# Kernel optimization log

Measured on AMD Instinct MI355X. Metric: run time of the kernel, lower is better.

## Reference

```python
import jax, jax.numpy as jnp
import numpy as np

NUM_EMBEDDINGS = 4096
EMBEDDING_DIM = 256
COMMITMENT_COST = 0.25
N_TOKENS = 32768


def setup_inputs() -> dict:
    key = jax.random.key(0)
    k1, k2 = jax.random.split(key)
    inputs = jax.random.normal(k1, (N_TOKENS, EMBEDDING_DIM), dtype=jnp.float32)
    # torch init: uniform(-1/K, 1/K)
    lim = 1.0 / NUM_EMBEDDINGS
    weight = jax.random.uniform(k2, (NUM_EMBEDDINGS, EMBEDDING_DIM), dtype=jnp.float32,
                                minval=-lim, maxval=lim)
    return {"inputs": inputs, "weight": weight}


def reference(inputs, weight):
    distances = (jnp.sum(inputs ** 2, axis=1, keepdims=True)
                 + jnp.sum(weight ** 2, axis=1)
                 - 2.0 * jnp.matmul(inputs, weight.T))
    encoding_indices = jnp.argmin(distances, axis=1)                       # [N]
    encodings = jax.nn.one_hot(encoding_indices, NUM_EMBEDDINGS,
                               dtype=jnp.float32)                          # [N, K]
    # gather replaces onehot @ weight (same values)
    quantized = weight[encoding_indices]                                   # [N, D]

    commitment_loss = jnp.mean((jax.lax.stop_gradient(quantized) - inputs) ** 2)
    codebook_loss = jnp.mean((quantized - jax.lax.stop_gradient(inputs)) ** 2)
    loss = codebook_loss + COMMITMENT_COST * commitment_loss

    # straight-through estimator
    quantized_st = inputs + jax.lax.stop_gradient(quantized - inputs)

    avg_probs = jnp.mean(encodings, axis=0)                                # [K]
    perplexity = jnp.exp(-jnp.sum(avg_probs * jnp.log(avg_probs + 1e-10)))

    return (quantized_st, perplexity, encodings, encoding_indices, loss)
```

## Files before the change

### kernel.cpp

```cpp
#include <hip/hip_runtime.h>

#define N_TOK 32768
#define N_EMB 4096
#define DIM 256

typedef short bf16x8 __attribute__((ext_vector_type(8)));
typedef float f32x4 __attribute__((ext_vector_type(4)));
typedef unsigned short us8 __attribute__((ext_vector_type(8)));


static __device__ __forceinline__ unsigned short f2bf(float f) {
    unsigned int u = __float_as_uint(f);
    u = (u + 0x7fffu + ((u >> 16) & 1u)) >> 16;
    return (unsigned short)u;
}

__device__ __forceinline__ float pw128_sq(const float4* a4) {
#pragma clang fp contract(off)
    float4 v0 = a4[0], v1 = a4[1];
    float r0 = v0.x * v0.x, r1 = v0.y * v0.y, r2 = v0.z * v0.z, r3 = v0.w * v0.w;
    float r4 = v1.x * v1.x, r5 = v1.y * v1.y, r6 = v1.z * v1.z, r7 = v1.w * v1.w;
    #pragma unroll
    for (int i = 1; i < 16; ++i) {
        v0 = a4[2 * i]; v1 = a4[2 * i + 1];
        float s;
        s = v0.x * v0.x; r0 += s;
        s = v0.y * v0.y; r1 += s;
        s = v0.z * v0.z; r2 += s;
        s = v0.w * v0.w; r3 += s;
        s = v1.x * v1.x; r4 += s;
        s = v1.y * v1.y; r5 += s;
        s = v1.z * v1.z; r6 += s;
        s = v1.w * v1.w; r7 += s;
    }
    return ((r0 + r1) + (r2 + r3)) + ((r4 + r5) + (r6 + r7));
}

__global__ __launch_bounds__(256) void k_norm_np(const float* __restrict__ src,
                                                 float* __restrict__ dst, int nrows) {
#pragma clang fp contract(off)
    int row = blockIdx.x * 256 + threadIdx.x;
    if (row >= nrows) return;
    const float4* a = (const float4*)(src + (size_t)row * DIM);
    float lo = pw128_sq(a);
    float hi = pw128_sq(a + 32);
    dst[row] = lo + hi;
}

__global__ __launch_bounds__(256) void k_shuf1(const float* __restrict__ src,
                                               unsigned short* __restrict__ hi) {
    int tid = blockIdx.x * 256 + threadIdx.x;
    int b = tid >> 6, lane = tid & 63;
    int T = b >> 3, C = b & 7;
    int row = T * 16 + (lane & 15);
    int col = C * 32 + (lane >> 4) * 8;
    const float* s = src + (size_t)row * DIM + col;
    us8 h;
    #pragma unroll
    for (int j = 0; j < 8; ++j) h[j] = f2bf(s[j]);
    *(us8*)(hi + (size_t)tid * 8) = h;
}

__global__ __launch_bounds__(256, 4) void k_score_mfma(
        const float* __restrict__ x, const float* __restrict__ w,
        const float* __restrict__ e2_np, const float* __restrict__ x2_np,
        const unsigned short* __restrict__ Xh,
        const unsigned short* __restrict__ Wh,
        float* __restrict__ out_idx, unsigned int* __restrict__ counts,
        float* enc,
        float* __restrict__ outq, float* __restrict__ loss_acc) {
    __shared__ __align__(16) short Abuf[8192];
    __shared__ float Tmax[4][32];
    __shared__ unsigned int ccnt[32];
    __shared__ int clist[32][16];
    __shared__ float Red_d[32 * 8];
    __shared__ int   Red_i[32 * 8];
    __shared__ float sred[4];

    const int t = threadIdx.x;
    const int wave = t >> 6, lane = t & 63;
    const int tok0 = blockIdx.x * 32;
    const int q = lane >> 4, c = lane & 15;

    #pragma unroll
    for (int i = 0; i < 4; ++i) {
        int idx = wave * 4 + i;
        int tile = idx >> 3, C = idx & 7;
        int Tg = blockIdx.x * 2 + tile;
        const unsigned short* src = Xh + ((size_t)(Tg * 8 + C) * 64 + lane) * 8;
        __builtin_amdgcn_global_load_lds(
            (const __attribute__((address_space(1))) unsigned int*)src,
            (__attribute__((address_space(3))) unsigned int*)(Abuf + idx * 512),
            16, 0, 0);
    }
    if (t < 32) ccnt[t] = 0;
    __syncthreads();

    f32x4* ez = enc ? (f32x4*)(enc + (size_t)tok0 * N_EMB) : (f32x4*)0;
    const f32x4 zf4 = {0.f, 0.f, 0.f, 0.f};

    float vmax[8], v2[8];
    #pragma unroll
    for (int s = 0; s < 8; ++s) { vmax[s] = -3.4e38f; v2[s] = -3.4e38f; }
    for (int jt = 0; jt < N_EMB; jt += 256) {
        const int U0 = (jt >> 4) + wave * 4;
        f32x4 acc[2][4] = {};
        #pragma unroll
        for (int C = 0; C < 8; ++C) {
            bf16x8 ah[2], bh[4];
            #pragma unroll
            for (int m = 0; m < 2; ++m)
                ah[m] = *(const bf16x8*)(Abuf + (size_t)(m * 8 + C) * 512 + lane * 8);
            #pragma unroll
            for (int n = 0; n < 4; ++n)
                bh[n] = *(const bf16x8*)(Wh + (((size_t)(U0 + n) * 8 + C) * 64 + lane) * 8);
            #pragma unroll
            for (int m = 0; m < 2; ++m)
                #pragma unroll
                for (int n = 0; n < 4; ++n)
                    acc[m][n] = __builtin_amdgcn_mfma_f32_16x16x32_bf16(ah[m], bh[n], acc[m][n], 0, 0, 0);
        }
        {
            unsigned int idb = ((unsigned int)jt >> 8) << 2;
            #pragma unroll
            for (int m = 0; m < 2; ++m)
                #pragma unroll
                for (int n = 0; n < 4; ++n)
                    #pragma unroll
                    for (int r = 0; r < 4; ++r) {
                        float p = __uint_as_float(
                            (__float_as_uint(acc[m][n][r]) & ~63u) | (idb + (unsigned)n));
                        int s = m * 4 + r;
                        if (p > vmax[s]) { v2[s] = vmax[s]; vmax[s] = p; }
                        else if (p > v2[s]) v2[s] = p;
                    }
        }
        if (ez) {
            int base = (jt >> 8) * 8 * 256 + t;
            #pragma unroll
            for (int j = 0; j < 8; ++j)
                __builtin_nontemporal_store(zf4, ez + base + j * 256);
        }
    }
    float rmax[8];
    #pragma unroll
    for (int s = 0; s < 8; ++s) rmax[s] = vmax[s];
    #pragma unroll
    for (int off = 1; off < 16; off <<= 1)
        #pragma unroll
        for (int s = 0; s < 8; ++s)
            rmax[s] = fmaxf(rmax[s], __shfl_xor(rmax[s], off));
    if (c == 0) {
        #pragma unroll
        for (int m = 0; m < 2; ++m)
            #pragma unroll
            for (int r = 0; r < 4; ++r)
                Tmax[wave][m * 16 + q * 4 + r] = rmax[m * 4 + r];
    }
    __syncthreads();
    if (t < 32) {
        float mx = fmaxf(fmaxf(Tmax[0][t], Tmax[1][t]),
                         fmaxf(Tmax[2][t], Tmax[3][t]));
        Tmax[0][t] = mx - 1.5e-4f;
    }
    __syncthreads();
    float thr[8];
    #pragma unroll
    for (int m = 0; m < 2; ++m)
        #pragma unroll
        for (int r = 0; r < 4; ++r)
            thr[m * 4 + r] = Tmax[0][m * 16 + q * 4 + r];

    #pragma unroll
    for (int s = 0; s < 8; ++s) {
        int m = s >> 2, r = s & 3;
        int tokl = m * 16 + q * 4 + r;
        #pragma unroll
        for (int h = 0; h < 2; ++h) {
            float pv = h ? v2[s] : vmax[s];
            if (pv >= thr[s]) {
                unsigned int id = __float_as_uint(pv) & 63u;
                int code = ((int)(id >> 2) * 16 + wave * 4 + (int)(id & 3u)) * 16 + c;
                unsigned int p = atomicAdd(&ccnt[tokl], 1u);
                if (p < 16) clist[tokl][p] = code;
            }
        }
    }
    __syncthreads();

    {
        int token = t >> 3, slot = t & 7;
        int cnt = (int)ccnt[token]; if (cnt > 16) cnt = 16;
        float bd = 3.4e38f;
        int bi = 0x7fffffff;
        float x2 = x2_np[tok0 + token];
        const float4* xr = (const float4*)(x + (size_t)(tok0 + token) * DIM);
        for (int k = slot; k < cnt; k += 8) {
            int code = clist[token][k];
            const float4* wr = (const float4*)(w + (size_t)code * DIM);
            double dot = 0.0;
            for (int g = 0; g < 64; ++g) {
                float4 xv = xr[g];
                float4 wv = wr[g];
                dot += (double)xv.x * (double)wv.x;
                dot += (double)xv.y * (double)wv.y;
                dot += (double)xv.z * (double)wv.z;
                dot += (double)xv.w * (double)wv.w;
            }
            {
#pragma clang fp contract(off)
                float M  = (float)dot;
                float S  = x2 + e2_np[code];
                float dd = S - 2.0f * M;
                if (dd < bd || (dd == bd && code < bi)) { bd = dd; bi = code; }
            }
        }
        Red_d[token * 8 + slot] = bd;
        Red_i[token * 8 + slot] = bi;
    }
    __syncthreads();
    if (t < 32) {
        float fv = Red_d[t * 8];
        int   fi = Red_i[t * 8];
        #pragma unroll
        for (int k = 1; k < 8; ++k) {
            float v = Red_d[t * 8 + k];
            int  ii = Red_i[t * 8 + k];
            if (v < fv || (v == fv && ii < fi)) { fv = v; fi = ii; }
        }
        out_idx[tok0 + t] = (float)fi;
        atomicAdd(&counts[fi], 1u);
        ccnt[t] = (unsigned int)fi;
    }
    __syncthreads();

    {
        int token = t >> 3, slot = t & 7;
        int fi = (int)ccnt[token];
        if (enc && slot == 0)
            __builtin_nontemporal_store(1.0f, enc + (size_t)(tok0 + token) * N_EMB + fi);
        const f32x4* wr = (const f32x4*)(w + (size_t)fi * DIM);
        const f32x4* xr = (const f32x4*)(x + (size_t)(tok0 + token) * DIM);
        f32x4* oq = (f32x4*)(outq + (size_t)(tok0 + token) * DIM);
        float sse = 0.f;
        #pragma unroll
        for (int g0 = 0; g0 < 8; ++g0) {
            int g = slot * 8 + g0;
            f32x4 qv = wr[g];
            f32x4 xv = xr[g];
            __builtin_nontemporal_store(qv, oq + g);
            float dx = qv.x - xv.x, dy = qv.y - xv.y;
            float dz = qv.z - xv.z, dw = qv.w - xv.w;
            sse += dx * dx + dy * dy + dz * dz + dw * dw;
        }
        #pragma unroll
        for (int off = 32; off > 0; off >>= 1) sse += __shfl_down(sse, off, 64);
        if (lane == 0) sred[wave] = sse;
    }
    __syncthreads();
    if (t == 0)
        atomicAdd(loss_acc, sred[0] + sred[1] + sred[2] + sred[3]);
}

__global__ __launch_bounds__(256) void k_onehot(const float* __restrict__ out_idx,
                                                float* __restrict__ enc) {
    int token = blockIdx.x;
    int idx = (int)out_idx[token];
    float4* row = (float4*)(enc + (size_t)token * N_EMB);
    #pragma unroll
    for (int p = 0; p < 4; ++p) {
        int g = threadIdx.x + 256 * p;
        float4 v = make_float4(0.f, 0.f, 0.f, 0.f);
        int d0 = g * 4;
        if (idx >= d0 && idx < d0 + 4) ((float*)&v)[idx - d0] = 1.0f;
        row[g] = v;
    }
}

__global__ __launch_bounds__(256) void k_final(const unsigned int* __restrict__ counts,
                                               const float* __restrict__ loss_acc,
                                               float* __restrict__ out_perp,
                                               float* __restrict__ out_loss) {
    __shared__ float sred[4];
    int t = threadIdx.x;
    float h = 0.f;
    for (int k = t; k < N_EMB; k += 256) {
        float p = (float)counts[k] * (1.0f / N_TOK);
        h += p * logf(p + 1e-10f);
    }
    #pragma unroll
    for (int off = 32; off > 0; off >>= 1) h += __shfl_down(h, off, 64);
    if ((t & 63) == 0) sred[t >> 6] = h;
    __syncthreads();
    if (t == 0) {
        float s = sred[0] + sred[1] + sred[2] + sred[3];
        *out_perp = expf(-s);
        *out_loss = loss_acc[0] * 1.25f / 8388608.0f;
    }
}

extern "C" void kernel_launch(void* const* d_in, const int* in_sizes, int n_in,
                              void* d_out, int out_size, void* d_ws, size_t ws_size,
                              hipStream_t stream) {
    const float* x = (const float*)d_in[0];
    const float* w = (const float*)d_in[1];
    float* out  = (float*)d_out;
    float* out0 = out;
    float* out1 = out0 + 8388608;
    float* out2 = out1 + 1;
    float* out3 = out2 + 134217728;
    float* out4 = out3 + 32768;

    unsigned int* counts = (unsigned int*)d_ws;
    float* loss_acc = (float*)((char*)d_ws + 16384);
    float* e2_np    = (float*)((char*)d_ws + 16896);
    float* x2_np    = (float*)((char*)d_ws + 33280);

    bool big_ws = ws_size >= (size_t)(20u * 1024u * 1024u);
    unsigned short *Xh, *Wh;
    float* enc_arg;
    if (big_ws) {
        Xh = (unsigned short*)((char*)d_ws + (1u << 20));
        Wh = Xh + 8388608;
        enc_arg = out2;
    } else {
        uintptr_t sb = ((uintptr_t)out2 + 255) & ~(uintptr_t)255;
        Xh = (unsigned short*)sb;
        Wh = Xh + 8388608;
        enc_arg = nullptr;
    }

    hipMemsetAsync(d_ws, 0, 16640, stream);
    k_norm_np<<<N_EMB / 256, 256, 0, stream>>>(w, e2_np, N_EMB);
    k_norm_np<<<N_TOK / 256, 256, 0, stream>>>(x, x2_np, N_TOK);
    k_shuf1<<<N_TOK * DIM / 8 / 256, 256, 0, stream>>>(x, Xh);
    k_shuf1<<<N_EMB * DIM / 8 / 256, 256, 0, stream>>>(w, Wh);
    k_score_mfma<<<N_TOK / 32, 256, 0, stream>>>(x, w, e2_np, x2_np, Xh, Wh,
                                                 out3, counts, enc_arg,
                                                 out0, loss_acc);
    if (!big_ws)
        k_onehot<<<N_TOK, 256, 0, stream>>>(out3, out2);
    k_final<<<1, 256, 0, stream>>>(counts, loss_acc, out1, out4);
}
```

Measured before the change: 756.5 us.

## Fuse prep kernels, branchless top-2 tracking, move one-hot zeroing after scoring

Merges the two norm kernels and two bf16 shuffle kernels into one prep launch that converts a 16-row tile and computes the row norms in the same block. Replaces the per-element branchy top-2 update in the score loop with a branchless fmax/fmed3 network over four candidates at once. Moves the non-temporal zero stores of the one-hot output out of the MFMA loop into one burst after candidate selection. This trades launch overhead and branch divergence for some loss of overlap between the zeroing stores and the matrix work.

```diff
diff --git a/kernel.cpp b/kernel.cpp
--- a/kernel.cpp
+++ b/kernel.cpp
@@ -13,6 +13,10 @@
     unsigned int u = __float_as_uint(f);
     u = (u + 0x7fffu + ((u >> 16) & 1u)) >> 16;
     return (unsigned short)u;
+}
+
+static __device__ __forceinline__ float pkid(float x, unsigned int id) {
+    return __uint_as_float((__float_as_uint(x) & ~63u) | id);
 }
 
 __device__ __forceinline__ float pw128_sq(const float4* a4) {
@@ -36,29 +40,38 @@
     return ((r0 + r1) + (r2 + r3)) + ((r4 + r5) + (r6 + r7));
 }
 
-__global__ __launch_bounds__(256) void k_norm_np(const float* __restrict__ src,
-                                                 float* __restrict__ dst, int nrows) {
-#pragma clang fp contract(off)
-    int row = blockIdx.x * 256 + threadIdx.x;
-    if (row >= nrows) return;
-    const float4* a = (const float4*)(src + (size_t)row * DIM);
-    float lo = pw128_sq(a);
-    float hi = pw128_sq(a + 32);
-    dst[row] = lo + hi;
-}
-
-__global__ __launch_bounds__(256) void k_shuf1(const float* __restrict__ src,
-                                               unsigned short* __restrict__ hi) {
-    int tid = blockIdx.x * 256 + threadIdx.x;
-    int b = tid >> 6, lane = tid & 63;
-    int T = b >> 3, C = b & 7;
-    int row = T * 16 + (lane & 15);
-    int col = C * 32 + (lane >> 4) * 8;
-    const float* s = src + (size_t)row * DIM + col;
-    us8 h;
-    #pragma unroll
-    for (int j = 0; j < 8; ++j) h[j] = f2bf(s[j]);
-    *(us8*)(hi + (size_t)tid * 8) = h;
+__global__ __launch_bounds__(256) void k_prep(const float* __restrict__ x,
+                                              const float* __restrict__ w,
+                                              unsigned short* __restrict__ Xh,
+                                              unsigned short* __restrict__ Wh,
+                                              float* __restrict__ x2_np,
+                                              float* __restrict__ e2_np) {
+    int bid = blockIdx.x;
+    const float* src;
+    unsigned short* dst;
+    float* ndst;
+    int T;
+    if (bid < N_TOK / 16) { src = x; dst = Xh; ndst = x2_np; T = bid; }
+    else                  { src = w; dst = Wh; ndst = e2_np; T = bid - N_TOK / 16; }
+    const int t = threadIdx.x, lane = t & 63, g = t >> 6;
+    #pragma unroll
+    for (int cc = 0; cc < 2; ++cc) {
+        int C = g * 2 + cc;
+        int row = T * 16 + (lane & 15);
+        int col = C * 32 + (lane >> 4) * 8;
+        const float* s = src + (size_t)row * DIM + col;
+        us8 h;
+        #pragma unroll
+        for (int j = 0; j < 8; ++j) h[j] = f2bf(s[j]);
+        *(us8*)(dst + ((size_t)(T * 8 + C) * 64 + lane) * 8) = h;
+    }
+    if (t < 16) {
+        int row = T * 16 + t;
+        const float4* a = (const float4*)(src + (size_t)row * DIM);
+        float lo = pw128_sq(a);
+        float hi = pw128_sq(a + 32);
+        ndst[row] = lo + hi;
+    }
 }
 
 __global__ __launch_bounds__(256, 4) void k_score_mfma(
@@ -96,9 +109,6 @@
     if (t < 32) ccnt[t] = 0;
     __syncthreads();
 
-    f32x4* ez = enc ? (f32x4*)(enc + (size_t)tok0 * N_EMB) : (f32x4*)0;
-    const f32x4 zf4 = {0.f, 0.f, 0.f, 0.f};
-
     float vmax[8], v2[8];
     #pragma unroll
     for (int s = 0; s < 8; ++s) { vmax[s] = -3.4e38f; v2[s] = -3.4e38f; }
@@ -125,21 +135,19 @@
             #pragma unroll
             for (int m = 0; m < 2; ++m)
                 #pragma unroll
-                for (int n = 0; n < 4; ++n)
-                    #pragma unroll
-                    for (int r = 0; r < 4; ++r) {
-                        float p = __uint_as_float(
-                            (__float_as_uint(acc[m][n][r]) & ~63u) | (idb + (unsigned)n));
-                        int s = m * 4 + r;
-                        if (p > vmax[s]) { v2[s] = vmax[s]; vmax[s] = p; }
-                        else if (p > v2[s]) v2[s] = p;
-                    }
-        }
-        if (ez) {
-            int base = (jt >> 8) * 8 * 256 + t;
-            #pragma unroll
-            for (int j = 0; j < 8; ++j)
-                __builtin_nontemporal_store(zf4, ez + base + j * 256);
+                for (int r = 0; r < 4; ++r) {
+                    int s = m * 4 + r;
+                    float p0 = pkid(acc[m][0][r], idb + 0);
+                    float p1 = pkid(acc[m][1][r], idb + 1);
+                    float p2 = pkid(acc[m][2][r], idb + 2);
+                    float p3 = pkid(acc[m][3][r], idb + 3);
+                    float t1a = fmaxf(fmaxf(vmax[s], p0), p1);
+                    float t2a = __builtin_amdgcn_fmed3f(vmax[s], p0, p1);
+                    float t1b = fmaxf(fmaxf(v2[s], p2), p3);
+                    float t2b = __builtin_amdgcn_fmed3f(v2[s], p2, p3);
+                    vmax[s] = fmaxf(t1a, t1b);
+                    v2[s]   = fmaxf(fmaxf(fminf(t1a, t1b), t2a), t2b);
+                }
         }
     }
     float rmax[8];
@@ -187,6 +195,14 @@
         }
     }
     __syncthreads();
+
+    if (enc) {
+        f32x4* ezb = (f32x4*)(enc + (size_t)tok0 * N_EMB);
+        const f32x4 zf4 = {0.f, 0.f, 0.f, 0.f};
+        #pragma unroll
+        for (int j = 0; j < 128; ++j)
+            __builtin_nontemporal_store(zf4, ezb + t + j * 256);
+    }
 
     {
         int token = t >> 3, slot = t & 7;
@@ -331,10 +347,7 @@
     }
 
     hipMemsetAsync(d_ws, 0, 16640, stream);
-    k_norm_np<<<N_EMB / 256, 256, 0, stream>>>(w, e2_np, N_EMB);
-    k_norm_np<<<N_TOK / 256, 256, 0, stream>>>(x, x2_np, N_TOK);
-    k_shuf1<<<N_TOK * DIM / 8 / 256, 256, 0, stream>>>(x, Xh);
-    k_shuf1<<<N_EMB * DIM / 8 / 256, 256, 0, stream>>>(w, Wh);
+    k_prep<<<N_TOK / 16 + N_EMB / 16, 256, 0, stream>>>(x, w, Xh, Wh, x2_np, e2_np);
     k_score_mfma<<<N_TOK / 32, 256, 0, stream>>>(x, w, e2_np, x2_np, Xh, Wh,
                                                  out3, counts, enc_arg,
                                                  out0, loss_acc);
```

Measured after the change: 806.2 us. +6.6%, slower.
